# Performance work log

Hardware: AMD Instinct MI355X
Metric: run time of the kernel (lower is better)

Reference implementation:

```python
import jax, jax.numpy as jnp
import numpy as np


def conv1d(x, w, b, pad):
    # x: (B, Cin, T), w: (Cout, Cin, K), b: (Cout,)
    y = jax.lax.conv_general_dilated(x, w, window_strides=(1,), padding=[(pad, pad)],
                                     dimension_numbers=('NCH', 'OIH', 'NCH'))
    return y + b[None, :, None]


def setup_inputs() -> dict:
    key = jax.random.key(0)
    ks = jax.random.split(key, 16)
    B, Cmel, Ctxt, Catt, T1, T2 = 16, 80, 256, 80, 800, 200
    s = 0.05
    return {
        'queries': jax.random.normal(ks[0], (B, Cmel, T1), jnp.float32),
        'keys': jax.random.normal(ks[1], (B, Ctxt, T2), jnp.float32),
        'attn_prior': jax.random.uniform(ks[2], (B, T1, T2), jnp.float32),
        # key_proj: Conv1d(256->512,k=3,pad=1) -> ReLU -> Conv1d(512->80,k=1)
        'kw1': jax.random.normal(ks[3], (Ctxt * 2, Ctxt, 3), jnp.float32) * s,
        'kb1': jax.random.normal(ks[4], (Ctxt * 2,), jnp.float32) * s,
        'kw2': jax.random.normal(ks[5], (Catt, Ctxt * 2, 1), jnp.float32) * s,
        'kb2': jax.random.normal(ks[6], (Catt,), jnp.float32) * s,
        # query_proj (3xconv): 80->160 k3 -> ReLU -> 160->80 k1 -> ReLU -> 80->80 k1
        'qw1': jax.random.normal(ks[7], (Cmel * 2, Cmel, 3), jnp.float32) * s,
        'qb1': jax.random.normal(ks[8], (Cmel * 2,), jnp.float32) * s,
        'qw2': jax.random.normal(ks[9], (Cmel, Cmel * 2, 1), jnp.float32) * s,
        'qb2': jax.random.normal(ks[10], (Cmel,), jnp.float32) * s,
        'qw3': jax.random.normal(ks[11], (Catt, Cmel, 1), jnp.float32) * s,
        'qb3': jax.random.normal(ks[12], (Catt,), jnp.float32) * s,
    }


def reference(queries, keys, attn_prior, kw1, kb1, kw2, kb2, qw1, qb1, qw2, qb2, qw3, qb3):
    # key encoder
    k = jax.nn.relu(conv1d(keys, kw1, kb1, pad=1))
    k = conv1d(k, kw2, kb2, pad=0)                      # (B, Catt, T2)
    # query encoder ('3xconv')
    q = jax.nn.relu(conv1d(queries, qw1, qb1, pad=1))
    q = jax.nn.relu(conv1d(q, qw2, qb2, pad=0))
    q = conv1d(q, qw3, qb3, pad=0)                      # (B, Catt, T1)
    # L2 distance over channels: ||q||^2 + ||k||^2 - 2 q.k (same math as broadcast (q-k)^2 sum)
    q2 = jnp.sum(q * q, axis=1)                         # (B, T1)
    k2 = jnp.sum(k * k, axis=1)                         # (B, T2)
    qk = jnp.einsum('bct,bcs->bts', q, k)               # (B, T1, T2)
    attn = -0.0005 * (q2[:, :, None] + k2[:, None, :] - 2.0 * qk)[:, None]  # (B,1,T1,T2)
    attn = jax.nn.log_softmax(attn, axis=3) + jnp.log(attn_prior[:, None] + 1e-8)
    return attn
```

## Files before the change

### kernel.cpp

```cpp
#include <hip/hip_runtime.h>
#include <cstdint>
#include <cmath>

using short8  = __attribute__((ext_vector_type(8))) short;
using short4v = __attribute__((ext_vector_type(4))) short;
using floatx4 = __attribute__((ext_vector_type(4))) float;

__device__ __forceinline__ short f2bf(float f) {
  union { float f; unsigned u; } x; x.f = f;
  unsigned r = x.u + 0x7FFFu + ((x.u >> 16) & 1u);
  return (short)(r >> 16);
}

__global__ __launch_bounds__(256) void prep_kernel(
    const float* __restrict__ keys, const float* __restrict__ queries,
    const float* __restrict__ kw1, const float* __restrict__ kw2,
    const float* __restrict__ qw1, const float* __restrict__ qw2,
    const float* __restrict__ qw3,
    short* __restrict__ kT0, short* __restrict__ qT0,
    short* __restrict__ w1, short* __restrict__ w2, short* __restrict__ w3,
    short* __restrict__ w4, short* __restrict__ w5)
{
  const int bid = blockIdx.x, tid = threadIdx.x;
  __shared__ float xs[32][65];

  if (bid < 1136) {
    const float* src; short* dst; int CIN, T, CP, bx, by, b;
    if (bid < 512) {
      src = keys; dst = kT0; CIN = 256; T = 200; CP = 256;
      bx = bid & 3; by = (bid >> 2) & 7; b = bid >> 5;
    } else {
      int b2 = bid - 512;
      src = queries; dst = qT0; CIN = 80; T = 800; CP = 96;
      bx = b2 % 13; by = (b2 / 13) % 3; b = b2 / 39;
    }
    const int t0 = bx * 64, ci0 = by * 32;
    for (int i = tid; i < 32 * 64; i += 256) {
      int row = i >> 6, col = i & 63;
      float v = 0.f;
      if (ci0 + row < CIN && t0 + col < T)
        v = src[((size_t)b * CIN + ci0 + row) * T + t0 + col];
      xs[row][col] = v;
    }
    __syncthreads();
    int t = tid >> 2, c8 = (tid & 3) * 8;
    if (t0 + t < T) {
      short8 o;
      #pragma unroll
      for (int j = 0; j < 8; ++j) o[j] = f2bf(xs[c8 + j][t]);
      *(short8*)&dst[((size_t)b * T + t0 + t) * CP + ci0 + c8] = o;
    }
  } else {
    int blk = bid - 1136;
    const float* src; short* dst; int base;
    int CoP, CiP, Cout, CIN, K;
    if      (blk < 384) { src=kw1; dst=w1; base=0;   CoP=512; CiP=256; Cout=512; CIN=256; K=3; }
    else if (blk < 432) { src=kw2; dst=w2; base=384; CoP=96;  CiP=512; Cout=80;  CIN=512; K=1; }
    else if (blk < 486) { src=qw1; dst=w3; base=432; CoP=192; CiP=96;  Cout=160; CIN=80;  K=3; }
    else if (blk < 504) { src=qw2; dst=w4; base=486; CoP=96;  CiP=192; Cout=80;  CIN=160; K=1; }
    else                { src=qw3; dst=w5; base=504; CoP=96;  CiP=96;  Cout=80;  CIN=80;  K=1; }
    int tot = K * CoP * CiP;
    int b0 = (blk - base) * 1024;
    for (int e = 0; e < 4; ++e) {
      int gi = b0 + e * 256 + tid;
      if (gi < tot) {
        int dk  = gi / (CoP * CiP);
        int rem = gi - dk * (CoP * CiP);
        int co  = rem / CiP, ci = rem - (rem / CiP) * CiP;
        float v = (co < Cout && ci < CIN) ? src[((size_t)co * CIN + ci) * K + dk] : 0.f;
        dst[gi] = f2bf(v);
      }
    }
  }
}

__global__ __launch_bounds__(256) void conv_k3_kernel(
    const short* __restrict__ kT0, const short* __restrict__ qT0,
    const short* __restrict__ w1, const short* __restrict__ w3,
    const short* __restrict__ w4, const short* __restrict__ w5,
    const float* __restrict__ kb1, const float* __restrict__ qb1,
    const float* __restrict__ qb2, const float* __restrict__ qb3,
    short* __restrict__ kT1, short* __restrict__ qF)
{
  __shared__ __align__(16) short smem[25680];
  const int tid = threadIdx.x, wid = tid >> 6, lane = tid & 63;
  const int q = lane >> 4, m = lane & 15;
  short* xs = smem;

  if (blockIdx.x < 512) {
    const int blk = blockIdx.x;
    const int b = blk >> 5, co0 = ((blk >> 2) & 7) * 64, t0 = (blk & 3) * 64;
    const int wy = wid >> 1, wx = wid & 1;
    short* as = smem + 2640;

    floatx4 acc[2][2];
    #pragma unroll
    for (int i = 0; i < 2; ++i)
      #pragma unroll
      for (int j = 0; j < 2; ++j) acc[i][j] = (floatx4){0.f, 0.f, 0.f, 0.f};

    for (int c0 = 0; c0 < 8; ++c0) {
      __syncthreads();
      for (int i = tid; i < 66 * 4; i += 256) {
        int row = i >> 2, c8 = (i & 3) * 8;
        int t = t0 + row - 1;
        int4 v = {0, 0, 0, 0};
        if (t >= 0 && t < 200)
          v = *(const int4*)&kT0[((size_t)b * 200 + t) * 256 + c0 * 32 + c8];
        *(int4*)&xs[row * 40 + c8] = v;
      }
      for (int i = tid; i < 192 * 4; i += 256) {
        int row = i >> 2, c8 = (i & 3) * 8;
        int dk = row >> 6, co = row & 63;
        *(int4*)&as[row * 40 + c8] =
            *(const int4*)&w1[((size_t)(dk * 512 + co0 + co)) * 256 + c0 * 32 + c8];
      }
      __syncthreads();
      #pragma unroll
      for (int dk = 0; dk < 3; ++dk) {
        short8 fa0 = *(const short8*)&as[(dk * 64 + wy * 32 + m) * 40 + q * 8];
        short8 fa1 = *(const short8*)&as[(dk * 64 + wy * 32 + 16 + m) * 40 + q * 8];
        #pragma unroll
        for (int j = 0; j < 2; ++j) {
          short8 fb = *(const short8*)&xs[(wx * 32 + j * 16 + m + dk) * 40 + q * 8];
          acc[0][j] = __builtin_amdgcn_mfma_f32_16x16x32_bf16(fa0, fb, acc[0][j], 0, 0, 0);
          acc[1][j] = __builtin_amdgcn_mfma_f32_16x16x32_bf16(fa1, fb, acc[1][j], 0, 0, 0);
        }
      }
    }
    #pragma unroll
    for (int i = 0; i < 2; ++i) {
      #pragma unroll
      for (int j = 0; j < 2; ++j) {
        #pragma unroll
        for (int r = 0; r < 4; ++r) {
          int co = co0 + wy * 32 + i * 16 + q * 4 + r;
          int t  = t0 + wx * 32 + j * 16 + m;
          if (t < 200) {
            float v = fmaxf(acc[i][j][r] + kb1[co], 0.f);
            kT1[((size_t)b * 200 + t) * 512 + co] = f2bf(v);
          }
        }
      }
    }
  } else {
    const int qbid = blockIdx.x - 512;
    const int b = qbid / 13, t0 = (qbid % 13) * 64;
    short* y1c = smem + 2640;
    short* y2c = smem + 18000;

    floatx4 accq[3][4];
    #pragma unroll
    for (int f = 0; f < 3; ++f)
      #pragma unroll
      for (int tf = 0; tf < 4; ++tf) accq[f][tf] = (floatx4){0.f, 0.f, 0.f, 0.f};

    for (int c0 = 0; c0 < 3; ++c0) {
      __syncthreads();
      for (int i = tid; i < 66 * 4; i += 256) {
        int row = i >> 2, c8 = (i & 3) * 8;
        int t = t0 + row - 1;
        int4 v = {0, 0, 0, 0};
        if (t >= 0 && t < 800)
          v = *(const int4*)&qT0[((size_t)b * 800 + t) * 96 + c0 * 32 + c8];
        *(int4*)&xs[row * 40 + c8] = v;
      }
      __syncthreads();
      #pragma unroll
      for (int dk = 0; dk < 3; ++dk) {
        short8 fa[3];
        #pragma unroll
        for (int f = 0; f < 3; ++f)
          fa[f] = *(const short8*)&w3[((size_t)(dk * 192 + wid * 48 + f * 16 + m)) * 96
                                      + c0 * 32 + q * 8];
        #pragma unroll
        for (int tf = 0; tf < 4; ++tf) {
          short8 fb = *(const short8*)&xs[(tf * 16 + m + dk) * 40 + q * 8];
          #pragma unroll
          for (int f = 0; f < 3; ++f)
            accq[f][tf] = __builtin_amdgcn_mfma_f32_16x16x32_bf16(fa[f], fb, accq[f][tf], 0, 0, 0);
        }
      }
    }
    __syncthreads();
    #pragma unroll
    for (int f = 0; f < 3; ++f) {
      #pragma unroll
      for (int tf = 0; tf < 4; ++tf) {
        int co = wid * 48 + f * 16 + q * 4;
        int t  = tf * 16 + m;
        short4v o;
        #pragma unroll
        for (int r = 0; r < 4; ++r) {
          float bv = (co + r < 160) ? qb1[co + r] : 0.f;
          o[r] = f2bf(fmaxf(accq[f][tf][r] + bv, 0.f));
        }
        *(short4v*)&y1c[(co >> 5) * 2560 + t * 40 + (co & 31)] = o;
      }
    }
    __syncthreads();

    floatx4 acc2q[6];
    #pragma unroll
    for (int f = 0; f < 6; ++f) acc2q[f] = (floatx4){0.f, 0.f, 0.f, 0.f};
    #pragma unroll
    for (int c = 0; c < 6; ++c) {
      short8 fb = *(const short8*)&y1c[c * 2560 + (wid * 16 + m) * 40 + q * 8];
      #pragma unroll
      for (int f = 0; f < 6; ++f) {
        short8 fa = *(const short8*)&w4[((size_t)(f * 16 + m)) * 192 + c * 32 + q * 8];
        acc2q[f] = __builtin_amdgcn_mfma_f32_16x16x32_bf16(fa, fb, acc2q[f], 0, 0, 0);
      }
    }
    #pragma unroll
    for (int f = 0; f < 6; ++f) {
      int co = f * 16 + q * 4;
      int t  = wid * 16 + m;
      short4v o;
      #pragma unroll
      for (int r = 0; r < 4; ++r) {
        float bv = (co + r < 80) ? qb2[co + r] : 0.f;
        o[r] = f2bf(fmaxf(acc2q[f][r] + bv, 0.f));
      }
      *(short4v*)&y2c[(co >> 5) * 2560 + t * 40 + (co & 31)] = o;
    }
    __syncthreads();

    floatx4 acc3q[6];
    #pragma unroll
    for (int f = 0; f < 6; ++f) acc3q[f] = (floatx4){0.f, 0.f, 0.f, 0.f};
    #pragma unroll
    for (int c = 0; c < 3; ++c) {
      short8 fb = *(const short8*)&y2c[c * 2560 + (wid * 16 + m) * 40 + q * 8];
      #pragma unroll
      for (int f = 0; f < 6; ++f) {
        short8 fa = *(const short8*)&w5[((size_t)(f * 16 + m)) * 96 + c * 32 + q * 8];
        acc3q[f] = __builtin_amdgcn_mfma_f32_16x16x32_bf16(fa, fb, acc3q[f], 0, 0, 0);
      }
    }
    int t = t0 + wid * 16 + m;
    if (t < 800) {
      #pragma unroll
      for (int f = 0; f < 6; ++f) {
        int co = f * 16 + q * 4;
        short4v o;
        #pragma unroll
        for (int r = 0; r < 4; ++r) {
          float bv = (co + r < 80) ? qb3[co + r] : 0.f;
          o[r] = f2bf(acc3q[f][r] + bv);
        }
        *(short4v*)&qF[((size_t)b * 800 + t) * 96 + co] = o;
      }
    }
  }
}

__global__ __launch_bounds__(256) void kconv2_kernel(
    const short* __restrict__ kT1, const short* __restrict__ w2,
    const float* __restrict__ kb2, short* __restrict__ kF)
{
  const int blk = blockIdx.x;
  const int b = blk >> 2, t0 = (blk & 3) * 64;
  const int tid = threadIdx.x, wid = tid >> 6, lane = tid & 63;
  const int q = lane >> 4, m = lane & 15;
  const int t = t0 + wid * 16 + m;
  const bool tv = (t < 200);

  floatx4 acc[6];
  #pragma unroll
  for (int f = 0; f < 6; ++f) acc[f] = (floatx4){0.f, 0.f, 0.f, 0.f};

  #pragma unroll
  for (int c = 0; c < 16; ++c) {
    short8 fb;
    if (tv) fb = *(const short8*)&kT1[((size_t)b * 200 + t) * 512 + c * 32 + q * 8];
    else    fb = (short8){0,0,0,0,0,0,0,0};
    #pragma unroll
    for (int f = 0; f < 6; ++f) {
      short8 fa = *(const short8*)&w2[((size_t)(f * 16 + m)) * 512 + c * 32 + q * 8];
      acc[f] = __builtin_amdgcn_mfma_f32_16x16x32_bf16(fa, fb, acc[f], 0, 0, 0);
    }
  }
  if (tv) {
    #pragma unroll
    for (int f = 0; f < 6; ++f) {
      int co = f * 16 + q * 4;
      short4v o;
      #pragma unroll
      for (int r = 0; r < 4; ++r) {
        float bv = (co + r < 80) ? kb2[co + r] : 0.f;
        o[r] = f2bf(acc[f][r] + bv);
      }
      *(short4v*)&kF[((size_t)b * 200 + t) * 96 + co] = o;
    }
  }
}

__global__ __launch_bounds__(256) void attn_mfma(
    const short* __restrict__ qT, const short* __restrict__ kT,
    const float* __restrict__ prior, float* __restrict__ out)
{
  const int b = blockIdx.y, t1_0 = blockIdx.x * 64;
  const int tid = threadIdx.x, wid = tid >> 6, lane = tid & 63;
  const int q = lane >> 4, m = lane & 15;

  __shared__ __align__(16) short aq[64 * 104];
  __shared__ __align__(16) short bk[208 * 40];
  __shared__ float k2s[208];

  floatx4 acc[13];
  #pragma unroll
  for (int f = 0; f < 13; ++f) acc[f] = (floatx4){0.f, 0.f, 0.f, 0.f};

  for (int i = tid; i < 64 * 12; i += 256) {
    int row = i / 12, g = i - (i / 12) * 12;
    int4 v = {0, 0, 0, 0};
    if (t1_0 + row < 800)
      v = *(const int4*)&qT[((size_t)b * 800 + t1_0 + row) * 96 + g * 8];
    *(int4*)&aq[row * 104 + g * 8] = v;
  }

  float k2acc = 0.f;
  for (int c = 0; c < 3; ++c) {
    __syncthreads();
    for (int i = tid; i < 208 * 4; i += 256) {
      int row = i >> 2, g = i & 3;
      int4 v = {0, 0, 0, 0};
      if (row < 200)
        v = *(const int4*)&kT[((size_t)b * 200 + row) * 96 + c * 32 + g * 8];
      *(int4*)&bk[row * 40 + g * 8] = v;
    }
    __syncthreads();
    if (tid < 208) {
      #pragma unroll
      for (int g = 0; g < 4; ++g) {
        short8 s = *(const short8*)&bk[tid * 40 + g * 8];
        #pragma unroll
        for (int j = 0; j < 8; ++j) {
          union { unsigned u; float f; } x; x.u = ((unsigned)(unsigned short)s[j]) << 16;
          k2acc = fmaf(x.f, x.f, k2acc);
        }
      }
    }
    short8 fa = *(const short8*)&aq[(wid * 16 + m) * 104 + c * 32 + q * 8];
    #pragma unroll
    for (int f = 0; f < 13; ++f) {
      short8 fb = *(const short8*)&bk[(f * 16 + m) * 40 + q * 8];
      acc[f] = __builtin_amdgcn_mfma_f32_16x16x32_bf16(fa, fb, acc[f], 0, 0, 0);
    }
  }
  if (tid < 208) k2s[tid] = k2acc;
  __syncthreads();

  float k2v[13];
  #pragma unroll
  for (int f = 0; f < 13; ++f) k2v[f] = k2s[f * 16 + m];

  float mx[4] = {-INFINITY, -INFINITY, -INFINITY, -INFINITY};
  #pragma unroll
  for (int f = 0; f < 13; ++f) {
    bool valid = (f * 16 + m) < 200;
    #pragma unroll
    for (int r = 0; r < 4; ++r) {
      float v = valid ? (0.001f * acc[f][r] - 0.0005f * k2v[f]) : -INFINITY;
      acc[f][r] = v;
      mx[r] = fmaxf(mx[r], v);
    }
  }
  #pragma unroll
  for (int msk = 1; msk < 16; msk <<= 1)
    #pragma unroll
    for (int r = 0; r < 4; ++r) mx[r] = fmaxf(mx[r], __shfl_xor(mx[r], msk));
  float sm[4] = {0.f, 0.f, 0.f, 0.f};
  #pragma unroll
  for (int f = 0; f < 13; ++f)
    #pragma unroll
    for (int r = 0; r < 4; ++r) sm[r] += __expf(acc[f][r] - mx[r]);
  #pragma unroll
  for (int msk = 1; msk < 16; msk <<= 1)
    #pragma unroll
    for (int r = 0; r < 4; ++r) sm[r] += __shfl_xor(sm[r], msk);
  float lse[4];
  #pragma unroll
  for (int r = 0; r < 4; ++r) lse[r] = mx[r] + __logf(sm[r]);

  #pragma unroll
  for (int f = 0; f < 13; ++f) {
    int col = f * 16 + m;
    if (col < 200) {
      #pragma unroll
      for (int r = 0; r < 4; ++r) {
        int t1 = t1_0 + wid * 16 + q * 4 + r;
        if (t1 < 800) {
          size_t o = ((size_t)b * 800 + t1) * 200 + col;
          out[o] = acc[f][r] - lse[r] + __logf(prior[o] + 1e-8f);
        }
      }
    }
  }
}

extern "C" void kernel_launch(void* const* d_in, const int* in_sizes, int n_in,
                              void* d_out, int out_size, void* d_ws, size_t ws_size,
                              hipStream_t stream) {
  const float* queries = (const float*)d_in[0];
  const float* keys    = (const float*)d_in[1];
  const float* prior   = (const float*)d_in[2];
  const float* kw1 = (const float*)d_in[3];
  const float* kb1 = (const float*)d_in[4];
  const float* kw2 = (const float*)d_in[5];
  const float* kb2 = (const float*)d_in[6];
  const float* qw1 = (const float*)d_in[7];
  const float* qb1 = (const float*)d_in[8];
  const float* qw2 = (const float*)d_in[9];
  const float* qb2 = (const float*)d_in[10];
  const float* qw3 = (const float*)d_in[11];
  const float* qb3 = (const float*)d_in[12];
  float* out = (float*)d_out;

  short* p = (short*)d_ws;
  short* kT0 = p;  p += (size_t)3200 * 256;
  short* qT0 = p;  p += (size_t)12800 * 96;
  short* w1  = p;  p += (size_t)3 * 512 * 256;
  short* w2  = p;  p += (size_t)96 * 512;
  short* w3  = p;  p += (size_t)3 * 192 * 96;
  short* w4  = p;  p += (size_t)96 * 192;
  short* w5  = p;  p += (size_t)96 * 96;
  short* kT1 = p;  p += (size_t)3200 * 512;
  short* kF  = p;  p += (size_t)3200 * 96;
  short* qF  = p;  p += (size_t)12800 * 96;

  prep_kernel<<<dim3(1649), 256, 0, stream>>>(keys, queries, kw1, kw2, qw1, qw2, qw3,
                                              kT0, qT0, w1, w2, w3, w4, w5);
  conv_k3_kernel<<<dim3(720), 256, 0, stream>>>(kT0, qT0, w1, w3, w4, w5,
                                                kb1, qb1, qb2, qb3, kT1, qF);
  kconv2_kernel<<<dim3(64), 256, 0, stream>>>(kT1, w2, kb2, kF);
  attn_mfma<<<dim3(13, 16), 256, 0, stream>>>(qF, kF, prior, out);
}
```

Baseline: 153.0 us.

## Stage attention output in LDS for coalesced vector stores; split kconv2 into smaller blocks

The attention kernel's epilogue now writes the normalized scores into a shared-memory staging buffer that reuses the Q/K tile space. It then reads prior and writes output as coalesced float4 rows, replacing the scattered per-element accesses from the MFMA register layout. The key 1x1 conv kernel now launches 208 single-wave blocks instead of 64 four-wave blocks to spread work across more CUs. The staging buffer enlarges LDS to 50 KB per block and adds two barriers, which may reduce occupancy.

```diff
diff --git a/kernel.cpp b/kernel.cpp
--- a/kernel.cpp
+++ b/kernel.cpp
@@ -255,15 +255,15 @@
   }
 }
 
-__global__ __launch_bounds__(256) void kconv2_kernel(
+__global__ __launch_bounds__(64) void kconv2_kernel(
     const short* __restrict__ kT1, const short* __restrict__ w2,
     const float* __restrict__ kb2, short* __restrict__ kF)
 {
   const int blk = blockIdx.x;
-  const int b = blk >> 2, t0 = (blk & 3) * 64;
-  const int tid = threadIdx.x, wid = tid >> 6, lane = tid & 63;
+  const int b = blk / 13, t0 = (blk - b * 13) * 16;
+  const int lane = threadIdx.x & 63;
   const int q = lane >> 4, m = lane & 15;
-  const int t = t0 + wid * 16 + m;
+  const int t = t0 + m;
   const bool tv = (t < 200);
 
   floatx4 acc[6];
@@ -304,9 +304,11 @@
   const int tid = threadIdx.x, wid = tid >> 6, lane = tid & 63;
   const int q = lane >> 4, m = lane & 15;
 
-  __shared__ __align__(16) short aq[64 * 104];
-  __shared__ __align__(16) short bk[208 * 40];
-  __shared__ float k2s[208];
+  __shared__ __align__(16) char smem[51200];
+  short* aq = (short*)smem;
+  short* bk = (short*)(smem + 13312);
+  float* k2s = (float*)(smem + 29952);
+  float* sstage = (float*)smem;
 
   floatx4 acc[13];
   #pragma unroll
@@ -384,18 +386,29 @@
   #pragma unroll
   for (int r = 0; r < 4; ++r) lse[r] = mx[r] + __logf(sm[r]);
 
+  __syncthreads();
   #pragma unroll
   for (int f = 0; f < 13; ++f) {
     int col = f * 16 + m;
     if (col < 200) {
       #pragma unroll
-      for (int r = 0; r < 4; ++r) {
-        int t1 = t1_0 + wid * 16 + q * 4 + r;
-        if (t1 < 800) {
-          size_t o = ((size_t)b * 800 + t1) * 200 + col;
-          out[o] = acc[f][r] - lse[r] + __logf(prior[o] + 1e-8f);
-        }
-      }
+      for (int r = 0; r < 4; ++r)
+        sstage[(wid * 16 + q * 4 + r) * 200 + col] = acc[f][r] - lse[r];
+    }
+  }
+  __syncthreads();
+
+  for (int i = tid; i < 64 * 50; i += 256) {
+    int row = i / 50, seg = i - (i / 50) * 50;
+    int t1 = t1_0 + row;
+    if (t1 < 800) {
+      size_t o = ((size_t)b * 800 + t1) * 200 + seg * 4;
+      floatx4 pv = *(const floatx4*)&prior[o];
+      floatx4 sv = *(const floatx4*)&sstage[row * 200 + seg * 4];
+      floatx4 ov;
+      #pragma unroll
+      for (int j = 0; j < 4; ++j) ov[j] = sv[j] + __logf(pv[j] + 1e-8f);
+      *(floatx4*)&out[o] = ov;
     }
   }
 }
@@ -434,6 +447,6 @@
                                               kT0, qT0, w1, w2, w3, w4, w5);
   conv_k3_kernel<<<dim3(720), 256, 0, stream>>>(kT0, qT0, w1, w3, w4, w5,
                                                 kb1, qb1, qb2, qb3, kT1, qF);
-  kconv2_kernel<<<dim3(64), 256, 0, stream>>>(kT1, w2, kb2, kF);
+  kconv2_kernel<<<dim3(208), 64, 0, stream>>>(kT1, w2, kb2, kF);
   attn_mfma<<<dim3(13, 16), 256, 0, stream>>>(qF, kF, prior, out);
 }
```

Measured after the change: 139.3 us. 1.1x faster.
